# Kernel optimization log

Measured on AMD Instinct MI355X. Metric: run time of the kernel, lower is better.

Reference implementation:

```python
import math
import jax, jax.numpy as jnp
from jax import lax
import numpy as np

LN_EPS = 1e-5
K = 3          # deform-conv kernel size
PAD = 1        # 'same' padding so offset map matches output resolution


def setup_inputs() -> dict:
    key = jax.random.key(0)
    ks = jax.random.split(key, 6)
    B, C, H, W, Co = 4, 256, 64, 64, 256
    x = jax.random.normal(ks[0], (B, C, H, W), jnp.float32)
    dwc_w = jax.random.normal(ks[1], (C, 1, K, K), jnp.float32) * 0.02
    ln_w = jnp.ones((C,), jnp.float32)
    ln_b = jnp.zeros((C,), jnp.float32)
    fcd_w = jax.random.normal(ks[2], (1, C, 1, 1), jnp.float32) * 0.02
    fca_w = jax.random.normal(ks[3], (1, C, 1, 1), jnp.float32) * 0.02
    fan_in = C * K * K
    dconv_w = jax.random.normal(ks[4], (Co, C, K, K), jnp.float32) / math.sqrt(fan_in)
    dconv_b = jnp.zeros((Co,), jnp.float32)
    return dict(x=x, dwc_w=dwc_w, ln_w=ln_w, ln_b=ln_b,
                fcd_w=fcd_w, fca_w=fca_w, dconv_w=dconv_w, dconv_b=dconv_b)


def _bilinear_sample(x, py, px):
    # x: [B,C,H,W]; py/px: [B,KK,H,W] float sample positions (zero-padded border)
    B, C, H, W = x.shape
    y0 = jnp.floor(py); x0 = jnp.floor(px)
    y1 = y0 + 1.0;      x1 = x0 + 1.0
    wy1 = py - y0; wy0 = 1.0 - wy1
    wx1 = px - x0; wx0 = 1.0 - wx1

    def gather(yy, xx):
        valid = ((yy >= 0) & (yy < H) & (xx >= 0) & (xx < W)).astype(x.dtype)
        iy = jnp.clip(yy, 0, H - 1).astype(jnp.int32)
        ix = jnp.clip(xx, 0, W - 1).astype(jnp.int32)
        # per-batch fancy gather -> [B,C,KK,H,W]
        v = jax.vmap(lambda img, a, b: img[:, a, b])(x, iy, ix)
        return v * valid[:, None]

    return (gather(y0, x0) * (wy0 * wx0)[:, None]
          + gather(y0, x1) * (wy0 * wx1)[:, None]
          + gather(y1, x0) * (wy1 * wx0)[:, None]
          + gather(y1, x1) * (wy1 * wx1)[:, None])


def reference(x, dwc_w, ln_w, ln_b, fcd_w, fca_w, dconv_w, dconv_b):
    B, C, H, W = x.shape
    KK = K * K
    # --- offset branch ---
    h = lax.conv_general_dilated(x, dwc_w, (1, 1), ((1, 1), (1, 1)),
                                 dimension_numbers=('NCHW', 'OIHW', 'NCHW'),
                                 feature_group_count=C)
    mu = h.mean(axis=1, keepdims=True)
    var = h.var(axis=1, keepdims=True)
    h = (h - mu) * lax.rsqrt(var + LN_EPS)
    h = h * ln_w[None, :, None, None] + ln_b[None, :, None, None]
    h = jax.nn.relu(h)
    r = jax.nn.relu(jnp.einsum('bchw,oc->bohw', h, fcd_w[:, :, 0, 0]))      # [B,1,H,W]
    t = jnp.einsum('bchw,oc->bohw', h, fca_w[:, :, 0, 0])
    theta = (t / (1.0 + jnp.abs(t))) * (math.pi / 180.0)                     # softsign * pi/180
    ox = r * jnp.cos(theta)
    oy = r * jnp.sin(theta)
    # torch code: offsets = cat([ox tiled KK, oy tiled KK], dim=1) -> [B,2KK,H,W]
    off = jnp.concatenate([jnp.tile(ox, (1, KK, 1, 1)), jnp.tile(oy, (1, KK, 1, 1))], axis=1)
    # torchvision DeformConv2d convention: channel 2k = dy, channel 2k+1 = dx
    dy = off[:, 0::2]   # [B,KK,H,W]
    dx = off[:, 1::2]
    # --- deformable sampling ---
    ky = jnp.repeat(jnp.arange(K), K).astype(x.dtype)   # kernel row per tap
    kx = jnp.tile(jnp.arange(K), K).astype(x.dtype)     # kernel col per tap
    py = (jnp.arange(H, dtype=x.dtype) - PAD)[None, None, :, None] + ky[None, :, None, None] + dy
    px = (jnp.arange(W, dtype=x.dtype) - PAD)[None, None, None, :] + kx[None, :, None, None] + dx
    sampled = _bilinear_sample(x, py, px)               # [B,C,KK,H,W]
    Co = dconv_w.shape[0]
    out = jnp.einsum('bckhw,ock->bohw', sampled, dconv_w.reshape(Co, C, KK))
    return out + dconv_b[None, :, None, None]
```

## Files before the change

### kernel.cpp

```cpp
#include <hip/hip_runtime.h>
#include <hip/hip_bf16.h>

#define B_   4
#define C_   256
#define CO_  256
#define H_   64
#define W_   64
#define HW_  4096

typedef __attribute__((ext_vector_type(8))) short short8;
typedef __attribute__((ext_vector_type(4))) float f32x4;
typedef __attribute__((ext_vector_type(2))) float f32x2;

static __device__ __forceinline__ unsigned short f2bf(float f) {
    unsigned u = __builtin_bit_cast(unsigned, f);
    unsigned r = (u + 0x7fffu + ((u >> 16) & 1u)) >> 16;
    return (unsigned short)r;
}
static __device__ __forceinline__ float bf2f(unsigned short s) {
    unsigned u = ((unsigned)s) << 16;
    return __builtin_bit_cast(float, u);
}
static __device__ __forceinline__ f32x2 pk_mul(f32x2 a, f32x2 b) {
    f32x2 d; asm("v_pk_mul_f32 %0, %1, %2" : "=v"(d) : "v"(a), "v"(b)); return d;
}
static __device__ __forceinline__ f32x2 pk_fma(f32x2 a, f32x2 b, f32x2 c) {
    f32x2 d; asm("v_pk_fma_f32 %0, %1, %2, %3" : "=v"(d) : "v"(a), "v"(b), "v"(c)); return d;
}
static __device__ __forceinline__ f32x2 pk_add(f32x2 a, f32x2 b) {
    f32x2 d; asm("v_pk_add_f32 %0, %1, %2" : "=v"(d) : "v"(a), "v"(b)); return d;
}
static __device__ __forceinline__ unsigned cvtpk(float a, float b) {
    unsigned r; asm("v_cvt_pk_bf16_f32 %0, %1, %2" : "=v"(r) : "v"(a), "v"(b)); return r;
}
static __device__ __forceinline__ f32x2 unpack_bf2(unsigned d) {
    f32x2 v;
    v.x = __builtin_bit_cast(float, d << 16);
    v.y = __builtin_bit_cast(float, d & 0xffff0000u);
    return v;
}

__global__ void k_transpose(const float* __restrict__ x, unsigned short* __restrict__ xT)
{
    __shared__ float t[32][132];
    int bid = blockIdx.x;
    int b   = bid >> 8;
    int rem = bid & 255;
    int hwT = rem >> 1, cT = rem & 1;
    int hw0 = hwT * 32, c0 = cT * 128;
    int tid = threadIdx.x;
    const float* src = x + (size_t)b * C_ * HW_;
    {
        int hw4 = (tid & 7) << 2;
        int cr  = tid >> 3;
#pragma unroll
        for (int it = 0; it < 4; ++it) {
            int c = cr + it * 32;
            f32x4 v = *(const f32x4*)(src + (size_t)(c0 + c) * HW_ + hw0 + hw4);
            t[hw4 + 0][c] = v.x;
            t[hw4 + 1][c] = v.y;
            t[hw4 + 2][c] = v.z;
            t[hw4 + 3][c] = v.w;
        }
    }
    __syncthreads();
    {
        int c8  = (tid & 15) << 3;
        int hwr = tid >> 4;
        unsigned short* dst = xT + (size_t)(((b << 12) + hw0) * 256) + c0 + c8;
#pragma unroll
        for (int it = 0; it < 2; ++it) {
            int hw = hwr + it * 16;
            f32x4 va = *(const f32x4*)&t[hw][c8];
            f32x4 vb = *(const f32x4*)&t[hw][c8 + 4];
            uint4 u;
            u.x = cvtpk(va.x, va.y);
            u.y = cvtpk(va.z, va.w);
            u.z = cvtpk(vb.x, vb.y);
            u.w = cvtpk(vb.z, vb.w);
            *(uint4*)(dst + (size_t)hw * 256) = u;
        }
    }
}

__global__ void k_packB(const float* __restrict__ w, unsigned short* __restrict__ Bt)
{
    int e = blockIdx.x * 256 + threadIdx.x;
    int j   = e & 7;
    int l4  = (e >> 3) & 3;
    int l15 = (e >> 5) & 15;
    int ks  = (e >> 9) & 7;
    int og  = (e >> 12) & 15;
    int k   = e >> 16;
    int o = og * 16 + l15;
    int c = ks * 32 + l4 * 8 + j;
    Bt[e] = f2bf(w[(o * C_ + c) * 9 + k]);
}

__launch_bounds__(512, 4)
__global__ void k_main(const unsigned short* __restrict__ xT,
                       const float* __restrict__ dwc_w,
                       const float* __restrict__ ln_w,
                       const float* __restrict__ ln_b,
                       const float* __restrict__ fcd_w,
                       const float* __restrict__ fca_w,
                       const unsigned short* __restrict__ Bt,
                       const float* __restrict__ bias,
                       float* __restrict__ out)
{
    __shared__ __align__(16) unsigned char smem[65536];

    int tid = threadIdx.x;
    int bi = blockIdx.x;
    int g = ((bi & 7) << 6) | (bi >> 3);
    int tile = g >> 1;
    int n0g = g & 1;
    int b = tile >> 6;
    int y = tile & 63;

    int lane = tid & 63, wid = tid >> 6;
    int l15 = lane & 15, l4 = lane >> 4;

    int gpos = tid >> 3;
    int csub = tid & 7;
    int ch0  = csub << 5;
    unsigned csub16 = (unsigned)csub << 4;
    const unsigned short* xb = xT + (size_t)b * HW_ * C_;
    const char* xbB = (const char*)xb;

    float* wsm = (float*)smem;
    for (int i = tid; i < 2304; i += 512) {
        int c = i / 9, j = i - c * 9;
        wsm[j * 256 + c] = dwc_w[i];
    }
    __syncthreads();

    float ox, oy;
    {
        f32x2 acc2[16];
#pragma unroll
        for (int i = 0; i < 16; ++i) { acc2[i].x = 0.f; acc2[i].y = 0.f; }
#pragma unroll
        for (int j = 0; j < 9; ++j) {
            int gy = y + j / 3 - 1, gx = gpos + j % 3 - 1;
            if (gy >= 0 && gy < H_ && gx >= 0 && gx < W_) {
                const unsigned short* p = xb + (size_t)((gy << 6) + gx) * 256 + ch0;
                const float* wrow = wsm + j * 256 + ch0;
#pragma unroll
                for (int cc = 0; cc < 4; ++cc) {
                    short8 r = *(const short8*)(p + cc * 8);
                    f32x4 wa = *(const f32x4*)(wrow + cc * 8);
                    f32x4 wb2 = *(const f32x4*)(wrow + cc * 8 + 4);
                    f32x2 wp0; wp0.x = wa.x; wp0.y = wa.y;
                    f32x2 wp1; wp1.x = wa.z; wp1.y = wa.w;
                    f32x2 wp2; wp2.x = wb2.x; wp2.y = wb2.y;
                    f32x2 wp3; wp3.x = wb2.z; wp3.y = wb2.w;
                    acc2[cc*4+0] = pk_fma(unpack_bf2(((unsigned*)&r)[0]), wp0, acc2[cc*4+0]);
                    acc2[cc*4+1] = pk_fma(unpack_bf2(((unsigned*)&r)[1]), wp1, acc2[cc*4+1]);
                    acc2[cc*4+2] = pk_fma(unpack_bf2(((unsigned*)&r)[2]), wp2, acc2[cc*4+2]);
                    acc2[cc*4+3] = pk_fma(unpack_bf2(((unsigned*)&r)[3]), wp3, acc2[cc*4+3]);
                }
            }
        }
        f32x2 sum2, sq2;
        sum2.x = 0.f; sum2.y = 0.f; sq2.x = 0.f; sq2.y = 0.f;
#pragma unroll
        for (int i = 0; i < 16; ++i) {
            sum2 = pk_add(sum2, acc2[i]);
            sq2  = pk_fma(acc2[i], acc2[i], sq2);
        }
        float s1 = sum2.x + sum2.y, s2 = sq2.x + sq2.y;
#pragma unroll
        for (int m = 1; m <= 4; m <<= 1) {
            s1 += __shfl_xor(s1, m);
            s2 += __shfl_xor(s2, m);
        }
        float mu  = s1 * (1.f / 256.f);
        float var = s2 * (1.f / 256.f) - mu * mu;
        float rs  = rsqrtf(var + 1e-5f);
        float d1 = 0.f, d2 = 0.f;
#pragma unroll
        for (int cc = 0; cc < 4; ++cc) {
            f32x4 lwa = *(const f32x4*)(ln_w  + ch0 + cc * 8);
            f32x4 lwb = *(const f32x4*)(ln_w  + ch0 + cc * 8 + 4);
            f32x4 lba = *(const f32x4*)(ln_b  + ch0 + cc * 8);
            f32x4 lbb = *(const f32x4*)(ln_b  + ch0 + cc * 8 + 4);
            f32x4 fda = *(const f32x4*)(fcd_w + ch0 + cc * 8);
            f32x4 fdb = *(const f32x4*)(fcd_w + ch0 + cc * 8 + 4);
            f32x4 faa = *(const f32x4*)(fca_w + ch0 + cc * 8);
            f32x4 fab = *(const f32x4*)(fca_w + ch0 + cc * 8 + 4);
#pragma unroll
            for (int i = 0; i < 8; ++i) {
                float av = (i & 1) ? acc2[cc*4 + (i >> 1)].y : acc2[cc*4 + (i >> 1)].x;
                float lw = (i < 4) ? lwa[i] : lwb[i - 4];
                float lb = (i < 4) ? lba[i] : lbb[i - 4];
                float fd = (i < 4) ? fda[i] : fdb[i - 4];
                float fa = (i < 4) ? faa[i] : fab[i - 4];
                float hn = (av - mu) * rs * lw + lb;
                hn = fmaxf(hn, 0.f);
                d1 = fmaf(hn, fd, d1);
                d2 = fmaf(hn, fa, d2);
            }
        }
#pragma unroll
        for (int m = 1; m <= 4; m <<= 1) {
            d1 += __shfl_xor(d1, m);
            d2 += __shfl_xor(d2, m);
        }
        float r0 = fmaxf(d1, 0.f);
        float theta = d2 / (1.f + fabsf(d2)) * 0.017453292519943295f;
        ox = r0 * cosf(theta);
        oy = r0 * sinf(theta);
    }
    __syncthreads();

    f32x4 acc[4];
#pragma unroll
    for (int m = 0; m < 4; ++m) {
        acc[m].x = 0.f; acc[m].y = 0.f; acc[m].z = 0.f; acc[m].w = 0.f;
    }

    const unsigned short* bwave = Bt + (unsigned)(n0g * 8 + wid) * 4096u
                                     + (unsigned)(l15 * 32 + l4 * 8);
    unsigned rowb = (unsigned)gpos * 512u;
    unsigned swzoff = (csub16 >> 4 ^ ((unsigned)gpos & 7u)) << 4;

#define GADDR(k)                                                                  \
        int ky = (k) / 3, kx = (k) - ky * 3;                                      \
        float dyv = ((k) <= 4) ? ox : oy;                                         \
        float dxv = ((k) <= 3) ? ox : oy;                                         \
        float py = (float)(y - 1 + ky) + dyv;                                     \
        float px = (float)(gpos - 1 + kx) + dxv;                                  \
        float y0f = floorf(py), x0f = floorf(px);                                 \
        int y0 = (int)y0f, x0 = (int)x0f;                                         \
        int y1 = y0 + 1, x1 = x0 + 1;                                             \
        float wy1 = py - y0f, wy0 = 1.f - wy1;                                    \
        float wx1 = px - x0f, wx0 = 1.f - wx1;                                    \
        float vy0 = (y0 >= 0 && y0 < H_) ? 1.f : 0.f;                             \
        float vy1 = (y1 >= 0 && y1 < H_) ? 1.f : 0.f;                             \
        float vx0 = (x0 >= 0 && x0 < W_) ? 1.f : 0.f;                             \
        float vx1 = (x1 >= 0 && x1 < W_) ? 1.f : 0.f;                             \
        w00 = wy0 * wx0 * vy0 * vx0; w01 = wy0 * wx1 * vy0 * vx1;                 \
        w10 = wy1 * wx0 * vy1 * vx0; w11 = wy1 * wx1 * vy1 * vx1;                 \
        int y0c = min(max(y0, 0), H_ - 1), y1c = min(max(y1, 0), H_ - 1);         \
        int x0c = min(max(x0, 0), W_ - 1), x1c = min(max(x1, 0), W_ - 1);         \
        o00 = (unsigned)((y0c << 6) + x0c) * 512u + csub16;                       \
        o01 = (unsigned)((y0c << 6) + x1c) * 512u + csub16;                       \
        o10 = (unsigned)((y1c << 6) + x0c) * 512u + csub16;                       \
        o11 = (unsigned)((y1c << 6) + x1c) * 512u + csub16;

#define GATHER_TAP(k, buf)                                                        \
    {   unsigned o00, o01, o10, o11;                                              \
        float w00, w01, w10, w11;                                                 \
        GADDR(k);                                                                 \
        f32x2 W00, W01, W10, W11;                                                 \
        W00.x = w00; W00.y = w00; W01.x = w01; W01.y = w01;                       \
        W10.x = w10; W10.y = w10; W11.x = w11; W11.y = w11;                       \
        unsigned wb = (unsigned)(buf) * 32768u + rowb + swzoff;                   \
        _Pragma("unroll")                                                         \
        for (int cq = 0; cq < 4; ++cq) {                                          \
            short8 r00 = *(const short8*)(xbB + o00 + cq * 128);                  \
            short8 r01 = *(const short8*)(xbB + o01 + cq * 128);                  \
            short8 r10 = *(const short8*)(xbB + o10 + cq * 128);                  \
            short8 r11 = *(const short8*)(xbB + o11 + cq * 128);                  \
            uint4 pkv;                                                            \
            _Pragma("unroll")                                                     \
            for (int dw = 0; dw < 4; ++dw) {                                      \
                f32x2 a2 = pk_mul(unpack_bf2(((unsigned*)&r00)[dw]), W00);        \
                a2 = pk_fma(unpack_bf2(((unsigned*)&r01)[dw]), W01, a2);          \
                a2 = pk_fma(unpack_bf2(((unsigned*)&r10)[dw]), W10, a2);          \
                a2 = pk_fma(unpack_bf2(((unsigned*)&r11)[dw]), W11, a2);          \
                ((unsigned*)&pkv)[dw] = cvtpk(a2.x, a2.y);                        \
            }                                                                     \
            *(uint4*)(smem + wb + cq * 128) = pkv;                                \
        }                                                                         \
    }

    GATHER_TAP(0, 0);
    __syncthreads();

#pragma unroll
    for (int k = 0; k < 9; ++k) {
        int t = k & 1;
        {
            const unsigned short* bk = bwave + (unsigned)k * 65536u;
            unsigned abase = (unsigned)t * 32768u;
#pragma unroll
            for (int ks = 0; ks < 8; ++ks) {
                short8 bf = *(const short8*)(bk + ks * 512);
                unsigned coff = (unsigned)(ks * 64 + (l4 << 4)) ^ (((unsigned)l15 & 7u) << 4);
#pragma unroll
                for (int mf = 0; mf < 4; ++mf) {
                    short8 a = *(const short8*)(smem + abase +
                                 (unsigned)(mf * 16 + l15) * 512u + coff);
                    acc[mf] = __builtin_amdgcn_mfma_f32_16x16x32_bf16(a, bf, acc[mf], 0, 0, 0);
                }
            }
        }
        if (k < 8) {
            GATHER_TAP(k + 1, t ^ 1);
        }
        __syncthreads();
    }

    float* epi = (float*)smem;
#pragma unroll
    for (int mf = 0; mf < 4; ++mf)
#pragma unroll
        for (int i = 0; i < 4; ++i) {
            int row = mf * 16 + l4 * 4 + i;
            int col = wid * 16 + l15;
            epi[row * 133 + col] = acc[mf][i];
        }
    __syncthreads();
    int o  = tid >> 2;
    int wq = (tid & 3) << 4;
    float bv = bias[n0g * 128 + o];
    float* orow = out + (size_t)(((b * CO_ + n0g * 128 + o) * H_ + y) * W_) + wq;
#pragma unroll
    for (int j = 0; j < 16; j += 4) {
        f32x4 v;
        v.x = epi[(wq + j + 0) * 133 + o] + bv;
        v.y = epi[(wq + j + 1) * 133 + o] + bv;
        v.z = epi[(wq + j + 2) * 133 + o] + bv;
        v.w = epi[(wq + j + 3) * 133 + o] + bv;
        *(f32x4*)(orow + j) = v;
    }
}

extern "C" void kernel_launch(void* const* d_in, const int* in_sizes, int n_in,
                              void* d_out, int out_size, void* d_ws, size_t ws_size,
                              hipStream_t stream) {
    const float* x      = (const float*)d_in[0];
    const float* dwc_w  = (const float*)d_in[1];
    const float* ln_w   = (const float*)d_in[2];
    const float* ln_b   = (const float*)d_in[3];
    const float* fcd_w  = (const float*)d_in[4];
    const float* fca_w  = (const float*)d_in[5];
    const float* dconv_w= (const float*)d_in[6];
    const float* dconv_b= (const float*)d_in[7];
    float* out = (float*)d_out;

    unsigned char* ws = (unsigned char*)d_ws;
    unsigned short* xT = (unsigned short*)(ws);
    unsigned short* Bt = (unsigned short*)(ws + 8388608);

    k_transpose<<<1024, 256, 0, stream>>>(x, xT);
    k_packB<<<2304, 256, 0, stream>>>(dconv_w, Bt);
    k_main<<<512, 512, 0, stream>>>(xT, dwc_w, ln_w, ln_b, fcd_w, fca_w, Bt, dconv_b, out);
}
```

Before: 81.98 us.

## Retile main kernel to 32 pixels by all output channels, dropping duplicated offset work

Before, each block handled 64 pixels for half the output channels, so the offset branch and the bilinear gather were done twice per row. Now each block takes 32 pixels and all 256 output channels, with each wave computing a 2x2 block of MFMA tiles. This removes the duplicated depthwise-conv, LayerNorm and gather work and halves shared memory use, which may allow more blocks per CU. The depthwise weights are transposed once inside the packing kernel and read from global memory instead of being staged in shared memory, which also removes a barrier. The cost is more B-fragment loads per wave and a larger epilogue stride.

```diff
diff --git a/kernel.cpp b/kernel.cpp
--- a/kernel.cpp
+++ b/kernel.cpp
@@ -16,10 +16,6 @@
     unsigned u = __builtin_bit_cast(unsigned, f);
     unsigned r = (u + 0x7fffu + ((u >> 16) & 1u)) >> 16;
     return (unsigned short)r;
-}
-static __device__ __forceinline__ float bf2f(unsigned short s) {
-    unsigned u = ((unsigned)s) << 16;
-    return __builtin_bit_cast(float, u);
 }
 static __device__ __forceinline__ f32x2 pk_mul(f32x2 a, f32x2 b) {
     f32x2 d; asm("v_pk_mul_f32 %0, %1, %2" : "=v"(d) : "v"(a), "v"(b)); return d;
@@ -83,9 +79,13 @@
     }
 }
 
-__global__ void k_packB(const float* __restrict__ w, unsigned short* __restrict__ Bt)
+__global__ void k_packB(const float* __restrict__ w, unsigned short* __restrict__ Bt,
+                        const float* __restrict__ dwc_w, float* __restrict__ dwcT)
 {
-    int e = blockIdx.x * 256 + threadIdx.x;
+    int bid = blockIdx.x;
+    int tid = threadIdx.x;
+    if (bid < 9) dwcT[bid * 256 + tid] = dwc_w[tid * 9 + bid];
+    int e = bid * 256 + tid;
     int j   = e & 7;
     int l4  = (e >> 3) & 3;
     int l15 = (e >> 5) & 15;
@@ -99,7 +99,7 @@
 
 __launch_bounds__(512, 4)
 __global__ void k_main(const unsigned short* __restrict__ xT,
-                       const float* __restrict__ dwc_w,
+                       const float* __restrict__ dwcT,
                        const float* __restrict__ ln_w,
                        const float* __restrict__ ln_b,
                        const float* __restrict__ fcd_w,
@@ -108,70 +108,60 @@
                        const float* __restrict__ bias,
                        float* __restrict__ out)
 {
-    __shared__ __align__(16) unsigned char smem[65536];
+    __shared__ __align__(16) unsigned char smem[33024];
 
     int tid = threadIdx.x;
     int bi = blockIdx.x;
     int g = ((bi & 7) << 6) | (bi >> 3);
-    int tile = g >> 1;
-    int n0g = g & 1;
-    int b = tile >> 6;
-    int y = tile & 63;
+    int p0 = g << 5;
+    int b = p0 >> 12;
+    int y = (p0 >> 6) & 63;
+    int xh = p0 & 63;
 
     int lane = tid & 63, wid = tid >> 6;
     int l15 = lane & 15, l4 = lane >> 4;
 
-    int gpos = tid >> 3;
-    int csub = tid & 7;
-    int ch0  = csub << 5;
-    unsigned csub16 = (unsigned)csub << 4;
+    int gpos = tid >> 4;
+    int csub = tid & 15;
     const unsigned short* xb = xT + (size_t)b * HW_ * C_;
     const char* xbB = (const char*)xb;
 
-    float* wsm = (float*)smem;
-    for (int i = tid; i < 2304; i += 512) {
-        int c = i / 9, j = i - c * 9;
-        wsm[j * 256 + c] = dwc_w[i];
-    }
-    __syncthreads();
-
     float ox, oy;
     {
-        f32x2 acc2[16];
-#pragma unroll
-        for (int i = 0; i < 16; ++i) { acc2[i].x = 0.f; acc2[i].y = 0.f; }
+        int ch0 = csub << 4;
+        f32x2 acc2[8];
+#pragma unroll
+        for (int i = 0; i < 8; ++i) { acc2[i].x = 0.f; acc2[i].y = 0.f; }
 #pragma unroll
         for (int j = 0; j < 9; ++j) {
-            int gy = y + j / 3 - 1, gx = gpos + j % 3 - 1;
+            int gy = y + j / 3 - 1, gx = xh + gpos + j % 3 - 1;
             if (gy >= 0 && gy < H_ && gx >= 0 && gx < W_) {
                 const unsigned short* p = xb + (size_t)((gy << 6) + gx) * 256 + ch0;
-                const float* wrow = wsm + j * 256 + ch0;
-#pragma unroll
-                for (int cc = 0; cc < 4; ++cc) {
-                    short8 r = *(const short8*)(p + cc * 8);
-                    f32x4 wa = *(const f32x4*)(wrow + cc * 8);
-                    f32x4 wb2 = *(const f32x4*)(wrow + cc * 8 + 4);
-                    f32x2 wp0; wp0.x = wa.x; wp0.y = wa.y;
-                    f32x2 wp1; wp1.x = wa.z; wp1.y = wa.w;
-                    f32x2 wp2; wp2.x = wb2.x; wp2.y = wb2.y;
-                    f32x2 wp3; wp3.x = wb2.z; wp3.y = wb2.w;
-                    acc2[cc*4+0] = pk_fma(unpack_bf2(((unsigned*)&r)[0]), wp0, acc2[cc*4+0]);
-                    acc2[cc*4+1] = pk_fma(unpack_bf2(((unsigned*)&r)[1]), wp1, acc2[cc*4+1]);
-                    acc2[cc*4+2] = pk_fma(unpack_bf2(((unsigned*)&r)[2]), wp2, acc2[cc*4+2]);
-                    acc2[cc*4+3] = pk_fma(unpack_bf2(((unsigned*)&r)[3]), wp3, acc2[cc*4+3]);
+                short8 rlo = *(const short8*)(p);
+                short8 rhi = *(const short8*)(p + 8);
+                const float* wrow = dwcT + j * 256 + ch0;
+#pragma unroll
+                for (int q = 0; q < 4; ++q) {
+                    f32x4 wv = *(const f32x4*)(wrow + q * 4);
+                    f32x2 w01v; w01v.x = wv.x; w01v.y = wv.y;
+                    f32x2 w23v; w23v.x = wv.z; w23v.y = wv.w;
+                    unsigned lo = (q < 2) ? ((unsigned*)&rlo)[q * 2] : ((unsigned*)&rhi)[(q - 2) * 2];
+                    unsigned hi = (q < 2) ? ((unsigned*)&rlo)[q * 2 + 1] : ((unsigned*)&rhi)[(q - 2) * 2 + 1];
+                    acc2[q * 2 + 0] = pk_fma(unpack_bf2(lo), w01v, acc2[q * 2 + 0]);
+                    acc2[q * 2 + 1] = pk_fma(unpack_bf2(hi), w23v, acc2[q * 2 + 1]);
                 }
             }
         }
         f32x2 sum2, sq2;
         sum2.x = 0.f; sum2.y = 0.f; sq2.x = 0.f; sq2.y = 0.f;
 #pragma unroll
-        for (int i = 0; i < 16; ++i) {
+        for (int i = 0; i < 8; ++i) {
             sum2 = pk_add(sum2, acc2[i]);
             sq2  = pk_fma(acc2[i], acc2[i], sq2);
         }
         float s1 = sum2.x + sum2.y, s2 = sq2.x + sq2.y;
 #pragma unroll
-        for (int m = 1; m <= 4; m <<= 1) {
+        for (int m = 1; m <= 8; m <<= 1) {
             s1 += __shfl_xor(s1, m);
             s2 += __shfl_xor(s2, m);
         }
@@ -180,30 +170,22 @@
         float rs  = rsqrtf(var + 1e-5f);
         float d1 = 0.f, d2 = 0.f;
 #pragma unroll
-        for (int cc = 0; cc < 4; ++cc) {
-            f32x4 lwa = *(const f32x4*)(ln_w  + ch0 + cc * 8);
-            f32x4 lwb = *(const f32x4*)(ln_w  + ch0 + cc * 8 + 4);
-            f32x4 lba = *(const f32x4*)(ln_b  + ch0 + cc * 8);
-            f32x4 lbb = *(const f32x4*)(ln_b  + ch0 + cc * 8 + 4);
-            f32x4 fda = *(const f32x4*)(fcd_w + ch0 + cc * 8);
-            f32x4 fdb = *(const f32x4*)(fcd_w + ch0 + cc * 8 + 4);
-            f32x4 faa = *(const f32x4*)(fca_w + ch0 + cc * 8);
-            f32x4 fab = *(const f32x4*)(fca_w + ch0 + cc * 8 + 4);
-#pragma unroll
-            for (int i = 0; i < 8; ++i) {
-                float av = (i & 1) ? acc2[cc*4 + (i >> 1)].y : acc2[cc*4 + (i >> 1)].x;
-                float lw = (i < 4) ? lwa[i] : lwb[i - 4];
-                float lb = (i < 4) ? lba[i] : lbb[i - 4];
-                float fd = (i < 4) ? fda[i] : fdb[i - 4];
-                float fa = (i < 4) ? faa[i] : fab[i - 4];
-                float hn = (av - mu) * rs * lw + lb;
+        for (int q = 0; q < 4; ++q) {
+            f32x4 lwv = *(const f32x4*)(ln_w  + ch0 + q * 4);
+            f32x4 lbv = *(const f32x4*)(ln_b  + ch0 + q * 4);
+            f32x4 fdv = *(const f32x4*)(fcd_w + ch0 + q * 4);
+            f32x4 fav = *(const f32x4*)(fca_w + ch0 + q * 4);
+#pragma unroll
+            for (int i = 0; i < 4; ++i) {
+                float av = (i & 1) ? acc2[q * 2 + (i >> 1)].y : acc2[q * 2 + (i >> 1)].x;
+                float hn = (av - mu) * rs * lwv[i] + lbv[i];
                 hn = fmaxf(hn, 0.f);
-                d1 = fmaf(hn, fd, d1);
-                d2 = fmaf(hn, fa, d2);
+                d1 = fmaf(hn, fdv[i], d1);
+                d2 = fmaf(hn, fav[i], d2);
             }
         }
 #pragma unroll
-        for (int m = 1; m <= 4; m <<= 1) {
+        for (int m = 1; m <= 8; m <<= 1) {
             d1 += __shfl_xor(d1, m);
             d2 += __shfl_xor(d2, m);
         }
@@ -212,25 +194,27 @@
         ox = r0 * cosf(theta);
         oy = r0 * sinf(theta);
     }
-    __syncthreads();
-
-    f32x4 acc[4];
-#pragma unroll
-    for (int m = 0; m < 4; ++m) {
-        acc[m].x = 0.f; acc[m].y = 0.f; acc[m].z = 0.f; acc[m].w = 0.f;
-    }
-
-    const unsigned short* bwave = Bt + (unsigned)(n0g * 8 + wid) * 4096u
+
+    f32x4 acc[2][2];
+#pragma unroll
+    for (int m = 0; m < 2; ++m)
+#pragma unroll
+        for (int n = 0; n < 2; ++n) {
+            acc[m][n].x = 0.f; acc[m][n].y = 0.f; acc[m][n].z = 0.f; acc[m][n].w = 0.f;
+        }
+
+    const unsigned short* bwave = Bt + (unsigned)(wid * 2) * 4096u
                                      + (unsigned)(l15 * 32 + l4 * 8);
     unsigned rowb = (unsigned)gpos * 512u;
-    unsigned swzoff = (csub16 >> 4 ^ ((unsigned)gpos & 7u)) << 4;
+    unsigned csub16 = (unsigned)csub << 4;
+    unsigned swzcol = csub16 ^ (((unsigned)gpos & 7u) << 4);
 
 #define GADDR(k)                                                                  \
         int ky = (k) / 3, kx = (k) - ky * 3;                                      \
         float dyv = ((k) <= 4) ? ox : oy;                                         \
         float dxv = ((k) <= 3) ? ox : oy;                                         \
         float py = (float)(y - 1 + ky) + dyv;                                     \
-        float px = (float)(gpos - 1 + kx) + dxv;                                  \
+        float px = (float)(xh + gpos - 1 + kx) + dxv;                             \
         float y0f = floorf(py), x0f = floorf(px);                                 \
         int y0 = (int)y0f, x0 = (int)x0f;                                         \
         int y1 = y0 + 1, x1 = x0 + 1;                                             \
@@ -256,13 +240,13 @@
         f32x2 W00, W01, W10, W11;                                                 \
         W00.x = w00; W00.y = w00; W01.x = w01; W01.y = w01;                       \
         W10.x = w10; W10.y = w10; W11.x = w11; W11.y = w11;                       \
-        unsigned wb = (unsigned)(buf) * 32768u + rowb + swzoff;                   \
+        unsigned wb = (unsigned)(buf) * 16384u + rowb + swzcol;                   \
         _Pragma("unroll")                                                         \
-        for (int cq = 0; cq < 4; ++cq) {                                          \
-            short8 r00 = *(const short8*)(xbB + o00 + cq * 128);                  \
-            short8 r01 = *(const short8*)(xbB + o01 + cq * 128);                  \
-            short8 r10 = *(const short8*)(xbB + o10 + cq * 128);                  \
-            short8 r11 = *(const short8*)(xbB + o11 + cq * 128);                  \
+        for (int cq = 0; cq < 2; ++cq) {                                          \
+            short8 r00 = *(const short8*)(xbB + o00 + cq * 256);                  \
+            short8 r01 = *(const short8*)(xbB + o01 + cq * 256);                  \
+            short8 r10 = *(const short8*)(xbB + o10 + cq * 256);                  \
+            short8 r11 = *(const short8*)(xbB + o11 + cq * 256);                  \
             uint4 pkv;                                                            \
             _Pragma("unroll")                                                     \
             for (int dw = 0; dw < 4; ++dw) {                                      \
@@ -272,7 +256,7 @@
                 a2 = pk_fma(unpack_bf2(((unsigned*)&r11)[dw]), W11, a2);          \
                 ((unsigned*)&pkv)[dw] = cvtpk(a2.x, a2.y);                        \
             }                                                                     \
-            *(uint4*)(smem + wb + cq * 128) = pkv;                                \
+            *(uint4*)(smem + wb + cq * 256) = pkv;                                \
         }                                                                         \
     }
 
@@ -284,17 +268,18 @@
         int t = k & 1;
         {
             const unsigned short* bk = bwave + (unsigned)k * 65536u;
-            unsigned abase = (unsigned)t * 32768u;
+            unsigned abase = (unsigned)t * 16384u;
 #pragma unroll
             for (int ks = 0; ks < 8; ++ks) {
-                short8 bf = *(const short8*)(bk + ks * 512);
+                short8 bf0 = *(const short8*)(bk + ks * 512);
+                short8 bf1 = *(const short8*)(bk + 4096 + ks * 512);
                 unsigned coff = (unsigned)(ks * 64 + (l4 << 4)) ^ (((unsigned)l15 & 7u) << 4);
-#pragma unroll
-                for (int mf = 0; mf < 4; ++mf) {
-                    short8 a = *(const short8*)(smem + abase +
-                                 (unsigned)(mf * 16 + l15) * 512u + coff);
-                    acc[mf] = __builtin_amdgcn_mfma_f32_16x16x32_bf16(a, bf, acc[mf], 0, 0, 0);
-                }
+                short8 a0 = *(const short8*)(smem + abase + (unsigned)l15 * 512u + coff);
+                short8 a1 = *(const short8*)(smem + abase + (unsigned)(16 + l15) * 512u + coff);
+                acc[0][0] = __builtin_amdgcn_mfma_f32_16x16x32_bf16(a0, bf0, acc[0][0], 0, 0, 0);
+                acc[0][1] = __builtin_amdgcn_mfma_f32_16x16x32_bf16(a0, bf1, acc[0][1], 0, 0, 0);
+                acc[1][0] = __builtin_amdgcn_mfma_f32_16x16x32_bf16(a1, bf0, acc[1][0], 0, 0, 0);
+                acc[1][1] = __builtin_amdgcn_mfma_f32_16x16x32_bf16(a1, bf1, acc[1][1], 0, 0, 0);
             }
         }
         if (k < 8) {
@@ -305,25 +290,27 @@
 
     float* epi = (float*)smem;
 #pragma unroll
-    for (int mf = 0; mf < 4; ++mf)
-#pragma unroll
-        for (int i = 0; i < 4; ++i) {
-            int row = mf * 16 + l4 * 4 + i;
-            int col = wid * 16 + l15;
-            epi[row * 133 + col] = acc[mf][i];
-        }
+    for (int m = 0; m < 2; ++m)
+#pragma unroll
+        for (int n = 0; n < 2; ++n)
+#pragma unroll
+            for (int i = 0; i < 4; ++i) {
+                int row = m * 16 + l4 * 4 + i;
+                int col = wid * 32 + n * 16 + l15;
+                epi[row * 257 + col] = acc[m][n][i];
+            }
     __syncthreads();
-    int o  = tid >> 2;
-    int wq = (tid & 3) << 4;
-    float bv = bias[n0g * 128 + o];
-    float* orow = out + (size_t)(((b * CO_ + n0g * 128 + o) * H_ + y) * W_) + wq;
+    int o  = tid >> 1;
+    int wq = (tid & 1) << 4;
+    float bv = bias[o];
+    float* orow = out + (size_t)(((b * CO_ + o) * H_ + y) * W_) + xh + wq;
 #pragma unroll
     for (int j = 0; j < 16; j += 4) {
         f32x4 v;
-        v.x = epi[(wq + j + 0) * 133 + o] + bv;
-        v.y = epi[(wq + j + 1) * 133 + o] + bv;
-        v.z = epi[(wq + j + 2) * 133 + o] + bv;
-        v.w = epi[(wq + j + 3) * 133 + o] + bv;
+        v.x = epi[(wq + j + 0) * 257 + o] + bv;
+        v.y = epi[(wq + j + 1) * 257 + o] + bv;
+        v.z = epi[(wq + j + 2) * 257 + o] + bv;
+        v.w = epi[(wq + j + 3) * 257 + o] + bv;
         *(f32x4*)(orow + j) = v;
     }
 }
@@ -344,8 +331,9 @@
     unsigned char* ws = (unsigned char*)d_ws;
     unsigned short* xT = (unsigned short*)(ws);
     unsigned short* Bt = (unsigned short*)(ws + 8388608);
+    float* dwcT        = (float*)(ws + 9568256);
 
     k_transpose<<<1024, 256, 0, stream>>>(x, xT);
-    k_packB<<<2304, 256, 0, stream>>>(dconv_w, Bt);
-    k_main<<<512, 512, 0, stream>>>(xT, dwc_w, ln_w, ln_b, fcd_w, fca_w, Bt, dconv_b, out);
-}
+    k_packB<<<2304, 256, 0, stream>>>(dconv_w, Bt, dwc_w, dwcT);
+    k_main<<<512, 512, 0, stream>>>(xT, dwcT, ln_w, ln_b, fcd_w, fca_w, Bt, dconv_b, out);
+}
```

Measured after the change: 78.08 us. 1.05x faster.
